# Kernel optimization log

Hardware: AMD Instinct MI355X
Metric: run time of the kernel (lower is better)

## Reference

```python
import jax, jax.numpy as jnp
import numpy as np

N_NODES = 100000
N_EDGES = 3200000
FEAT = 256
HIDDEN = 32
EMBED = 16


def gcn_conv(x, row, col, ew, W, b, num_nodes):
    """PyG GCNConv (add_self_loops=True, normalize=True) in eval mode.
    x: [N, Fin], row/col: [E] (source, target), ew: [E], W: [Fout, Fin], b: [Fout].
    """
    # add self loops with weight 1 (fill_value=1.0)
    loop = jnp.arange(num_nodes, dtype=row.dtype)
    row_f = jnp.concatenate([row, loop])
    col_f = jnp.concatenate([col, loop])
    ew_f = jnp.concatenate([ew, jnp.ones((num_nodes,), dtype=ew.dtype)])
    # symmetric normalization: deg over target (col) for source_to_target flow
    deg = jax.ops.segment_sum(ew_f, col_f, num_segments=num_nodes)
    dis = jnp.where(deg > 0, jax.lax.rsqrt(deg), 0.0)  # deg^{-1/2}, inf -> 0
    norm = dis[row_f] * ew_f * dis[col_f]  # [E+N]
    h = x @ W.T  # [N, Fout] -- linear (no bias) before propagate
    msg = h[row_f] * norm[:, None]  # gather + weight messages
    out = jax.ops.segment_sum(msg, col_f, num_segments=num_nodes)  # scatter-add
    return out + b


def setup_inputs() -> dict:
    key = jax.random.key(0)
    ks = jax.random.split(key, 8)
    x = jax.random.normal(ks[0], (N_NODES, FEAT), dtype=jnp.float32)
    ei = jax.random.randint(ks[1], (2, N_EDGES), 0, N_NODES, dtype=jnp.int64)
    ew = jax.random.uniform(ks[2], (N_EDGES,), dtype=jnp.float32)
    s1 = 1.0 / np.sqrt(FEAT)
    s2 = 1.0 / np.sqrt(HIDDEN)
    W1 = jax.random.uniform(ks[3], (HIDDEN, FEAT), minval=-s1, maxval=s1, dtype=jnp.float32)
    b1 = jax.random.uniform(ks[4], (HIDDEN,), minval=-s1, maxval=s1, dtype=jnp.float32)
    W2 = jax.random.uniform(ks[5], (EMBED, HIDDEN), minval=-s2, maxval=s2, dtype=jnp.float32)
    b2 = jax.random.uniform(ks[6], (EMBED,), minval=-s2, maxval=s2, dtype=jnp.float32)
    return {"x": x, "ei": ei, "ew": ew, "W1": W1, "b1": b1, "W2": W2, "b2": b2}


def reference(x, ei, ew, W1, b1, W2, b2):
    row, col = ei[0], ei[1]
    h = gcn_conv(x, row, col, ew, W1, b1, N_NODES)
    h = jax.nn.relu(h)
    # Dropout(0.25) and DropEdge(0.8) are identity in eval mode
    return gcn_conv(h, row, col, ew, W2, b2, N_NODES)
```

## Files before the change

### kernel.cpp

```cpp
#include <hip/hip_runtime.h>
#include <hip/hip_bf16.h>

#define N_NODES 100000
#define N_EDGES 3200000
#define FEAT 256
#define HIDDEN 32
#define EMBED 16
#define NPB 128
#define NBIN ((N_NODES + NPB - 1) / NPB)
#define CAPB 4608
#define OCAP 8192
#define GR 128
#define G1N 32
#define G1CAP 2048
#define G2N 64
#define G2CAP 3072
#define PEPB 3072
#define PBLK ((N_EDGES + PEPB - 1) / PEPB)
#define OMS 784
#define RPT 5
#define NSK (NPB * 8)

__global__ void k_zero(int* __restrict__ ocur) {
    if (threadIdx.x == 0 && blockIdx.x == 0) *ocur = 0;
}

__global__ __launch_bounds__(256, 4) void k_part(
        const int* __restrict__ row, const int* __restrict__ col,
        const float* __restrict__ ew, int* __restrict__ offm,
        int2* __restrict__ chunks) {
    __shared__ int2 sed[PEPB];
    __shared__ int shist[NBIN];
    __shared__ int scur[NBIN];
    const int tid = threadIdx.x;
    const int blk = blockIdx.x;
    const int e0 = blk * PEPB;
    const int ne = min(PEPB, N_EDGES - e0);

    for (int i = tid; i < NBIN; i += 256) shist[i] = 0;
    __syncthreads();
    for (int i = tid; i < ne; i += 256) atomicAdd(&shist[col[e0 + i] >> 7], 1);
    __syncthreads();
    int l[4];
    int s = 0;
#pragma unroll
    for (int k = 0; k < 4; ++k) {
        int b = tid * 4 + k;
        l[k] = (b < NBIN) ? shist[b] : 0;
        s += l[k];
    }
    scur[tid] = s;
    __syncthreads();
    for (int d = 1; d < 256; d <<= 1) {
        int t = (tid >= d) ? scur[tid - d] : 0;
        __syncthreads();
        scur[tid] += t;
        __syncthreads();
    }
    int ex = scur[tid] - s;
    __syncthreads();
#pragma unroll
    for (int k = 0; k < 4; ++k) {
        int b = tid * 4 + k;
        if (b < NBIN) {
            shist[b] = ex;
            scur[b] = ex;
            ex += l[k];
        }
    }
    __syncthreads();
    for (int b = tid; b < NBIN; b += 256) offm[blk * OMS + b] = shist[b];
    if (tid == 0) offm[blk * OMS + NBIN] = ne;
    for (int i = tid; i < ne; i += 256) {
        int e = e0 + i;
        int c = col[e];
        int b = c >> 7;
        int p = atomicAdd(&scur[b], 1);
        sed[p] = make_int2(((c & (NPB - 1)) << 17) | row[e], __float_as_int(ew[e]));
    }
    __syncthreads();
    for (int i = tid; i < ne; i += 256) chunks[(size_t)blk * PEPB + i] = sed[i];
}

__global__ __launch_bounds__(256) void k_build(
        const int* __restrict__ offm, const int2* __restrict__ chunks,
        int2* __restrict__ binned, float* __restrict__ deg,
        int2* __restrict__ off2, int* __restrict__ binTot,
        int* __restrict__ ocur, int4* __restrict__ olist) {
    __shared__ int2 se[CAPB];
    __shared__ int scnt[NSK], scur2[NSK];
    __shared__ float sdeg[NPB];
    __shared__ int spart[256];
    const int bin = blockIdx.x, tid = threadIdx.x;
    const size_t base = (size_t)bin * CAPB;

    for (int i = tid; i < NSK; i += 256) scnt[i] = 0;
    for (int i = tid; i < NPB; i += 256) sdeg[i] = 0.f;
    int st[RPT], ln[RPT];
    int s = 0;
#pragma unroll
    for (int r = 0; r < RPT; ++r) {
        int k = tid * RPT + r;
        int a = 0, b2 = 0;
        if (k < PBLK) {
            a = offm[k * OMS + bin];
            b2 = offm[k * OMS + bin + 1];
        }
        st[r] = a;
        ln[r] = b2 - a;
        s += ln[r];
    }
    spart[tid] = s;
    __syncthreads();
    for (int d = 1; d < 256; d <<= 1) {
        int t = (tid >= d) ? spart[tid - d] : 0;
        __syncthreads();
        spart[tid] += t;
        __syncthreads();
    }
    int ex = spart[tid] - s;
    const int nTot = spart[255];
    const int n = min(nTot, CAPB);
    int dp = ex;
#pragma unroll
    for (int r = 0; r < RPT; ++r) {
        int k = tid * RPT + r;
        if (k < PBLK) {
            const int2* src = chunks + (size_t)k * PEPB + st[r];
            for (int j = 0; j < ln[r]; ++j) {
                int2 v = src[j];
                int lc = v.x >> 17;
                int dst = dp + j;
                if (dst < CAPB) {
                    se[dst] = v;
                    atomicAdd(&scnt[lc * 8 + ((v.x & 0x1FFFF) >> 14)], 1);
                    atomicAdd(&sdeg[lc], __int_as_float(v.y));
                } else {
                    int q = atomicAdd(ocur, 1);
                    if (q < OCAP)
                        olist[q] = make_int4(v.x & 0x1FFFF, bin * NPB + lc, v.y, 0);
                }
            }
            dp += ln[r];
        }
    }
    __syncthreads();
    int l0 = scnt[tid * 4], l1 = scnt[tid * 4 + 1],
        l2 = scnt[tid * 4 + 2], l3 = scnt[tid * 4 + 3];
    int s2 = l0 + l1 + l2 + l3;
    spart[tid] = s2;
    __syncthreads();
    for (int d = 1; d < 256; d <<= 1) {
        int t = (tid >= d) ? spart[tid - d] : 0;
        __syncthreads();
        spart[tid] += t;
        __syncthreads();
    }
    int ex2 = spart[tid] - s2;
    scnt[tid * 4] = ex2;
    scnt[tid * 4 + 1] = ex2 + l0;
    scnt[tid * 4 + 2] = ex2 + l0 + l1;
    scnt[tid * 4 + 3] = ex2 + l0 + l1 + l2;
    __syncthreads();
    for (int i = tid; i < NSK; i += 256) scur2[i] = scnt[i];
    __syncthreads();
    if (tid < NPB) {
        int node = bin * NPB + tid;
        if (node < N_NODES) {
            int stn = scnt[tid * 8];
            int en = (tid == NPB - 1) ? n : scnt[(tid + 1) * 8];
            off2[node] = make_int2((int)base + stn, en - stn);
            deg[node] = sdeg[tid] + 1.0f;
        }
    }
    if (tid == 0) binTot[bin] = n;
    __syncthreads();
    for (int i = tid; i < n; i += 256) {
        int2 v = se[i];
        int lc = v.x >> 17, src2 = v.x & 0x1FFFF;
        int p = atomicAdd(&scur2[lc * 8 + (src2 >> 14)], 1);
        binned[base + p] = make_int2(src2, v.y);
    }
}

__global__ void k_degover(const int* __restrict__ ocur, const int4* __restrict__ olist,
                          float* __restrict__ deg) {
    int p = blockIdx.x * blockDim.x + threadIdx.x;
    int n = min(*ocur, OCAP);
    if (p < n) { int4 t = olist[p]; unsafeAtomicAdd(&deg[t.y], __int_as_float(t.z)); }
}

__global__ void k_dis(float* __restrict__ deg) {
    int i = blockIdx.x * blockDim.x + threadIdx.x;
    if (i < N_NODES) {
        float d = deg[i];
        deg[i] = (d > 0.0f) ? rsqrtf(d) : 0.0f;
    }
}

__global__ void k_wnorm(const int* __restrict__ binTot, int2* __restrict__ csr,
                        const float* __restrict__ dis) {
    int bin = blockIdx.x;
    int n = binTot[bin];
    size_t base = (size_t)bin * CAPB;
    for (int i = threadIdx.x; i < n; i += 256) {
        int2 v = csr[base + i];
        float w = __int_as_float(v.y) * dis[v.x];
        csr[base + i] = make_int2(v.x, __float_as_int(w));
    }
}

__global__ __launch_bounds__(256) void k_gemm1(
        const float* __restrict__ x, const float* __restrict__ W1,
        float* __restrict__ h) {
    __shared__ float sx[GR][36];
    __shared__ float sw[HIDDEN][260];

    const int tid = threadIdx.x;
    const size_t base = (size_t)blockIdx.x * GR;
    const float4* x4 = (const float4*)x;
    const float4* w4 = (const float4*)W1;
    const int rs = tid >> 3;
    const int ks = tid & 7;

    for (int i = tid; i < HIDDEN * 64; i += 256) {
        int f = i >> 6, kq = i & 63;
        *(float4*)&sw[f][kq * 4] = w4[f * 64 + kq];
    }
    float4 stg[4];
#pragma unroll
    for (int m = 0; m < 4; ++m) {
        int rr = rs + 32 * m;
        stg[m] = make_float4(0.f, 0.f, 0.f, 0.f);
        if (base + rr < N_NODES) stg[m] = x4[(base + rr) * 64 + ks];
    }
#pragma unroll
    for (int m = 0; m < 4; ++m) *(float4*)&sx[rs + 32 * m][ks * 4] = stg[m];
    __syncthreads();

    const int r0 = tid >> 3;
    const int c0 = tid & 7;
    float acc[4][4] = {};

    for (int p = 0; p < 8; ++p) {
        if (p < 7) {
#pragma unroll
            for (int m = 0; m < 4; ++m) {
                int rr = rs + 32 * m;
                stg[m] = make_float4(0.f, 0.f, 0.f, 0.f);
                if (base + rr < N_NODES) stg[m] = x4[(base + rr) * 64 + (p + 1) * 8 + ks];
            }
        }
#pragma unroll
        for (int kq = 0; kq < 8; ++kq) {
            float4 xa[4], wv[4];
#pragma unroll
            for (int m = 0; m < 4; ++m) xa[m] = *(const float4*)&sx[r0 + 32 * m][kq * 4];
#pragma unroll
            for (int j = 0; j < 4; ++j) wv[j] = *(const float4*)&sw[c0 + 8 * j][(p * 8 + kq) * 4];
#pragma unroll
            for (int m = 0; m < 4; ++m)
#pragma unroll
                for (int j = 0; j < 4; ++j)
                    acc[m][j] += xa[m].x * wv[j].x + xa[m].y * wv[j].y +
                                 xa[m].z * wv[j].z + xa[m].w * wv[j].w;
        }
        __syncthreads();
        if (p < 7) {
#pragma unroll
            for (int m = 0; m < 4; ++m) *(float4*)&sx[rs + 32 * m][ks * 4] = stg[m];
            __syncthreads();
        }
    }

#pragma unroll
    for (int m = 0; m < 4; ++m) {
        size_t r = base + r0 + 32 * m;
        if (r < N_NODES) {
#pragma unroll
            for (int j = 0; j < 4; ++j) h[r * HIDDEN + c0 + 8 * j] = acc[m][j];
        }
    }
}

__global__ __launch_bounds__(256) void k_gather1(
        const int2* __restrict__ off2, const int2* __restrict__ csr,
        const float* __restrict__ h, const float* __restrict__ dis,
        const float* __restrict__ b1, float* __restrict__ out1) {
    __shared__ int2 sc[G1CAP];
    __shared__ int s_start, s_n;
    const int tid = threadIdx.x;
    const int node0 = blockIdx.x * G1N;
    if (tid == 0) {
        int2 a = off2[node0];
        int2 b = off2[node0 + G1N - 1];
        s_start = a.x;
        s_n = b.x + b.y - a.x;
    }
    __syncthreads();
    const int start = s_start, n = s_n;
    const bool fit = (n <= G1CAP);
    if (fit) for (int i = tid; i < n; i += 256) sc[i] = csr[start + i];
    __syncthreads();

    const int node = node0 + (tid >> 3);
    const int og = tid & 7;
    float d = dis[node];
    float d2 = d * d;
    float4 self = *(const float4*)(h + (size_t)node * HIDDEN + og * 4);
    float4 bv = *(const float4*)(b1 + og * 4);
    float4 acc = make_float4(0.f, 0.f, 0.f, 0.f);

    int2 o = off2[node];
    for (int j = 0; j < o.y; ++j) {
        int2 v = fit ? sc[o.x - start + j] : csr[o.x + j];
        float w = __int_as_float(v.y);
        const float4 hv = *(const float4*)(h + (size_t)v.x * HIDDEN + og * 4);
        acc.x += hv.x * w; acc.y += hv.y * w; acc.z += hv.z * w; acc.w += hv.w * w;
    }
    *(float4*)(out1 + (size_t)node * HIDDEN + og * 4) =
        make_float4(acc.x * d + self.x * d2 + bv.x, acc.y * d + self.y * d2 + bv.y,
                    acc.z * d + self.z * d2 + bv.z, acc.w * d + self.w * d2 + bv.w);
}

__global__ void k_over1(const int* __restrict__ ocur, const int4* __restrict__ olist,
                        const float* __restrict__ dis, const float* __restrict__ h,
                        float* __restrict__ out1) {
    int p = blockIdx.x * blockDim.x + threadIdx.x;
    int n = min(*ocur, OCAP);
    if (p < n) {
        int4 t = olist[p];
        int r = t.x, c = t.y;
        float w = dis[r] * __int_as_float(t.z) * dis[c];
        for (int f = 0; f < HIDDEN; ++f)
            unsafeAtomicAdd(&out1[(size_t)c * HIDDEN + f], h[(size_t)r * HIDDEN + f] * w);
    }
}

__global__ void k_gemm2(const float* __restrict__ out1, const float* __restrict__ W2,
                        float* __restrict__ h2) {
    int t = blockIdx.x * blockDim.x + threadIdx.x;
    int i = t >> 4;
    if (i >= N_NODES) return;
    int f = t & 15;
    const float* r = out1 + (size_t)i * HIDDEN;
    const float* w = W2 + f * HIDDEN;
    float acc = 0.f;
#pragma unroll
    for (int k = 0; k < HIDDEN; ++k) acc += fmaxf(r[k], 0.f) * w[k];
    h2[(size_t)i * EMBED + f] = acc;
}

__global__ __launch_bounds__(256) void k_gather2(
        const int2* __restrict__ off2, const int2* __restrict__ csr,
        const float* __restrict__ h2, const float* __restrict__ dis,
        const float* __restrict__ b2, float* __restrict__ out) {
    __shared__ int2 sc[G2CAP];
    __shared__ int s_start, s_n;
    const int tid = threadIdx.x;
    const int node0 = blockIdx.x * G2N;
    const int lastn = min(node0 + G2N, N_NODES) - 1;
    if (tid == 0) {
        int2 a = off2[node0];
        int2 b = off2[lastn];
        s_start = a.x;
        s_n = b.x + b.y - a.x;
    }
    __syncthreads();
    const int start = s_start, n = s_n;
    const bool fit = (n <= G2CAP);
    if (fit) for (int i = tid; i < n; i += 256) sc[i] = csr[start + i];
    __syncthreads();

    const int node = node0 + (tid >> 2);
    const int og = tid & 3;
    if (node >= N_NODES) return;
    float d = dis[node];
    float d2 = d * d;
    float4 self = *(const float4*)(h2 + (size_t)node * EMBED + og * 4);
    float4 bv = *(const float4*)(b2 + og * 4);
    float4 acc = make_float4(0.f, 0.f, 0.f, 0.f);

    int2 o = off2[node];
    for (int j = 0; j < o.y; ++j) {
        int2 v = fit ? sc[o.x - start + j] : csr[o.x + j];
        float w = __int_as_float(v.y);
        const float4 hv = *(const float4*)(h2 + (size_t)v.x * EMBED + og * 4);
        acc.x += hv.x * w; acc.y += hv.y * w; acc.z += hv.z * w; acc.w += hv.w * w;
    }
    *(float4*)(out + (size_t)node * EMBED + og * 4) =
        make_float4(acc.x * d + self.x * d2 + bv.x, acc.y * d + self.y * d2 + bv.y,
                    acc.z * d + self.z * d2 + bv.z, acc.w * d + self.w * d2 + bv.w);
}

__global__ void k_over2(const int* __restrict__ ocur, const int4* __restrict__ olist,
                        const float* __restrict__ dis, const float* __restrict__ h2,
                        float* __restrict__ out) {
    int p = blockIdx.x * blockDim.x + threadIdx.x;
    int n = min(*ocur, OCAP);
    if (p < n) {
        int4 t = olist[p];
        int r = t.x, c = t.y;
        float w = dis[r] * __int_as_float(t.z) * dis[c];
        for (int f = 0; f < EMBED; ++f)
            unsafeAtomicAdd(&out[(size_t)c * EMBED + f], h2[(size_t)r * EMBED + f] * w);
    }
}

extern "C" void kernel_launch(void* const* d_in, const int* in_sizes, int n_in,
                              void* d_out, int out_size, void* d_ws, size_t ws_size,
                              hipStream_t stream) {
    const float* x  = (const float*)d_in[0];
    const int*   ei = (const int*)d_in[1];
    const float* ew = (const float*)d_in[2];
    const float* W1 = (const float*)d_in[3];
    const float* b1 = (const float*)d_in[4];
    const float* W2 = (const float*)d_in[5];
    const float* b2 = (const float*)d_in[6];
    float* out = (float*)d_out;

    const int* row = ei;
    const int* col = ei + N_EDGES;

    int2*  off2   = (int2*)d_ws;
    int2*  binned = off2 + N_NODES;
    float* deg    = (float*)(binned + (size_t)NBIN * CAPB);
    int*   binTot = (int*)(deg + N_NODES);
    int*   offm   = binTot + 784;
    int*   ocur   = offm + (size_t)PBLK * OMS;
    int4*  olist  = (int4*)(ocur + 4);
    void*  big    = (void*)(olist + OCAP);
    int2*  chunks = (int2*)big;
    float* h      = (float*)big;
    float* out1   = h + (size_t)N_NODES * HIDDEN;
    float* h2     = h;

    const int B = 256;
    const int gN = (N_NODES + B - 1) / B;
    const int gO = (OCAP + B - 1) / B;

    k_zero<<<1, 64, 0, stream>>>(ocur);
    k_part<<<PBLK, B, 0, stream>>>(row, col, ew, offm, chunks);
    k_build<<<NBIN, B, 0, stream>>>(offm, chunks, binned, deg, off2, binTot, ocur, olist);
    k_degover<<<gO, B, 0, stream>>>(ocur, olist, deg);
    k_dis<<<gN, B, 0, stream>>>(deg);
    k_wnorm<<<NBIN, B, 0, stream>>>(binTot, binned, deg);
    k_gemm1<<<(N_NODES + GR - 1) / GR, B, 0, stream>>>(x, W1, h);
    k_gather1<<<N_NODES / G1N, B, 0, stream>>>(off2, binned, h, deg, b1, out1);
    k_over1<<<gO, B, 0, stream>>>(ocur, olist, deg, h, out1);
    k_gemm2<<<(N_NODES * 16 + B - 1) / B, B, 0, stream>>>(out1, W2, h2);
    k_gather2<<<(N_NODES + G2N - 1) / G2N, B, 0, stream>>>(off2, binned, h2, deg, b2, out);
    k_over2<<<gO, B, 0, stream>>>(ocur, olist, deg, h2, out);
}
```

Measured before the change: 329.1 us.

## Fuse overflow edges, ReLU and second GEMM into gather kernels

Layer 1's gather kernel now adds the overflow-list edges itself, applies ReLU, and multiplies by W2 through shared memory to write h2 directly. This removes the out1 round trip and the separate overflow-atomic and gemm2 launches. Layer 2's gather also folds in the overflow edges, so k_over2 is gone. In exchange, every thread scans the whole overflow list linearly whenever it is non-empty, which could be expensive if the list is large.

```diff
diff --git a/kernel.cpp b/kernel.cpp
--- a/kernel.cpp
+++ b/kernel.cpp
@@ -286,9 +286,13 @@
 __global__ __launch_bounds__(256) void k_gather1(
         const int2* __restrict__ off2, const int2* __restrict__ csr,
         const float* __restrict__ h, const float* __restrict__ dis,
-        const float* __restrict__ b1, float* __restrict__ out1) {
+        const float* __restrict__ b1, const float* __restrict__ W2,
+        const int* __restrict__ ocur, const int4* __restrict__ olist,
+        float* __restrict__ h2) {
     __shared__ int2 sc[G1CAP];
-    __shared__ int s_start, s_n;
+    __shared__ float sw2[EMBED][HIDDEN];
+    __shared__ float sout[G1N][HIDDEN + 1];
+    __shared__ int s_start, s_n, s_ov;
     const int tid = threadIdx.x;
     const int node0 = blockIdx.x * G1N;
     if (tid == 0) {
@@ -296,9 +300,11 @@
         int2 b = off2[node0 + G1N - 1];
         s_start = a.x;
         s_n = b.x + b.y - a.x;
-    }
-    __syncthreads();
-    const int start = s_start, n = s_n;
+        s_ov = *ocur;
+    }
+    if (tid < 128) ((float4*)sw2)[tid] = ((const float4*)W2)[tid];
+    __syncthreads();
+    const int start = s_start, n = s_n, ov = min(s_ov, OCAP);
     const bool fit = (n <= G1CAP);
     if (fit) for (int i = tid; i < n; i += 256) sc[i] = csr[start + i];
     __syncthreads();
@@ -318,45 +324,45 @@
         const float4 hv = *(const float4*)(h + (size_t)v.x * HIDDEN + og * 4);
         acc.x += hv.x * w; acc.y += hv.y * w; acc.z += hv.z * w; acc.w += hv.w * w;
     }
-    *(float4*)(out1 + (size_t)node * HIDDEN + og * 4) =
-        make_float4(acc.x * d + self.x * d2 + bv.x, acc.y * d + self.y * d2 + bv.y,
-                    acc.z * d + self.z * d2 + bv.z, acc.w * d + self.w * d2 + bv.w);
-}
-
-__global__ void k_over1(const int* __restrict__ ocur, const int4* __restrict__ olist,
-                        const float* __restrict__ dis, const float* __restrict__ h,
-                        float* __restrict__ out1) {
-    int p = blockIdx.x * blockDim.x + threadIdx.x;
-    int n = min(*ocur, OCAP);
-    if (p < n) {
-        int4 t = olist[p];
-        int r = t.x, c = t.y;
-        float w = dis[r] * __int_as_float(t.z) * dis[c];
-        for (int f = 0; f < HIDDEN; ++f)
-            unsafeAtomicAdd(&out1[(size_t)c * HIDDEN + f], h[(size_t)r * HIDDEN + f] * w);
-    }
-}
-
-__global__ void k_gemm2(const float* __restrict__ out1, const float* __restrict__ W2,
-                        float* __restrict__ h2) {
-    int t = blockIdx.x * blockDim.x + threadIdx.x;
-    int i = t >> 4;
-    if (i >= N_NODES) return;
-    int f = t & 15;
-    const float* r = out1 + (size_t)i * HIDDEN;
-    const float* w = W2 + f * HIDDEN;
-    float acc = 0.f;
-#pragma unroll
-    for (int k = 0; k < HIDDEN; ++k) acc += fmaxf(r[k], 0.f) * w[k];
-    h2[(size_t)i * EMBED + f] = acc;
+    float4 res = make_float4(acc.x * d + self.x * d2 + bv.x,
+                             acc.y * d + self.y * d2 + bv.y,
+                             acc.z * d + self.z * d2 + bv.z,
+                             acc.w * d + self.w * d2 + bv.w);
+    if (ov > 0) {
+        for (int q = 0; q < ov; ++q) {
+            int4 t = olist[q];
+            if (t.y == node) {
+                float w = dis[t.x] * __int_as_float(t.z) * d;
+                const float4 hv = *(const float4*)(h + (size_t)t.x * HIDDEN + og * 4);
+                res.x += hv.x * w; res.y += hv.y * w;
+                res.z += hv.z * w; res.w += hv.w * w;
+            }
+        }
+    }
+    *(float4*)&sout[tid >> 3][og * 4] =
+        make_float4(fmaxf(res.x, 0.f), fmaxf(res.y, 0.f),
+                    fmaxf(res.z, 0.f), fmaxf(res.w, 0.f));
+    __syncthreads();
+    const int n2 = tid >> 3;
+    const int f2 = (tid & 7) * 2;
+    float a0 = 0.f, a1 = 0.f;
+#pragma unroll
+    for (int k = 0; k < HIDDEN; ++k) {
+        float r = sout[n2][k];
+        a0 += r * sw2[f2][k];
+        a1 += r * sw2[f2 + 1][k];
+    }
+    h2[(size_t)(node0 + n2) * EMBED + f2] = a0;
+    h2[(size_t)(node0 + n2) * EMBED + f2 + 1] = a1;
 }
 
 __global__ __launch_bounds__(256) void k_gather2(
         const int2* __restrict__ off2, const int2* __restrict__ csr,
         const float* __restrict__ h2, const float* __restrict__ dis,
-        const float* __restrict__ b2, float* __restrict__ out) {
+        const float* __restrict__ b2, const int* __restrict__ ocur,
+        const int4* __restrict__ olist, float* __restrict__ out) {
     __shared__ int2 sc[G2CAP];
-    __shared__ int s_start, s_n;
+    __shared__ int s_start, s_n, s_ov;
     const int tid = threadIdx.x;
     const int node0 = blockIdx.x * G2N;
     const int lastn = min(node0 + G2N, N_NODES) - 1;
@@ -365,9 +371,10 @@
         int2 b = off2[lastn];
         s_start = a.x;
         s_n = b.x + b.y - a.x;
-    }
-    __syncthreads();
-    const int start = s_start, n = s_n;
+        s_ov = *ocur;
+    }
+    __syncthreads();
+    const int start = s_start, n = s_n, ov = min(s_ov, OCAP);
     const bool fit = (n <= G2CAP);
     if (fit) for (int i = tid; i < n; i += 256) sc[i] = csr[start + i];
     __syncthreads();
@@ -388,23 +395,22 @@
         const float4 hv = *(const float4*)(h2 + (size_t)v.x * EMBED + og * 4);
         acc.x += hv.x * w; acc.y += hv.y * w; acc.z += hv.z * w; acc.w += hv.w * w;
     }
-    *(float4*)(out + (size_t)node * EMBED + og * 4) =
-        make_float4(acc.x * d + self.x * d2 + bv.x, acc.y * d + self.y * d2 + bv.y,
-                    acc.z * d + self.z * d2 + bv.z, acc.w * d + self.w * d2 + bv.w);
-}
-
-__global__ void k_over2(const int* __restrict__ ocur, const int4* __restrict__ olist,
-                        const float* __restrict__ dis, const float* __restrict__ h2,
-                        float* __restrict__ out) {
-    int p = blockIdx.x * blockDim.x + threadIdx.x;
-    int n = min(*ocur, OCAP);
-    if (p < n) {
-        int4 t = olist[p];
-        int r = t.x, c = t.y;
-        float w = dis[r] * __int_as_float(t.z) * dis[c];
-        for (int f = 0; f < EMBED; ++f)
-            unsafeAtomicAdd(&out[(size_t)c * EMBED + f], h2[(size_t)r * EMBED + f] * w);
-    }
+    float4 res = make_float4(acc.x * d + self.x * d2 + bv.x,
+                             acc.y * d + self.y * d2 + bv.y,
+                             acc.z * d + self.z * d2 + bv.z,
+                             acc.w * d + self.w * d2 + bv.w);
+    if (ov > 0) {
+        for (int q = 0; q < ov; ++q) {
+            int4 t = olist[q];
+            if (t.y == node) {
+                float w = dis[t.x] * __int_as_float(t.z) * d;
+                const float4 hv = *(const float4*)(h2 + (size_t)t.x * EMBED + og * 4);
+                res.x += hv.x * w; res.y += hv.y * w;
+                res.z += hv.z * w; res.w += hv.w * w;
+            }
+        }
+    }
+    *(float4*)(out + (size_t)node * EMBED + og * 4) = res;
 }
 
 extern "C" void kernel_launch(void* const* d_in, const int* in_sizes, int n_in,
@@ -432,8 +438,7 @@
     void*  big    = (void*)(olist + OCAP);
     int2*  chunks = (int2*)big;
     float* h      = (float*)big;
-    float* out1   = h + (size_t)N_NODES * HIDDEN;
-    float* h2     = h;
+    float* h2     = h + (size_t)N_NODES * HIDDEN;
 
     const int B = 256;
     const int gN = (N_NODES + B - 1) / B;
@@ -446,9 +451,6 @@
     k_dis<<<gN, B, 0, stream>>>(deg);
     k_wnorm<<<NBIN, B, 0, stream>>>(binTot, binned, deg);
     k_gemm1<<<(N_NODES + GR - 1) / GR, B, 0, stream>>>(x, W1, h);
-    k_gather1<<<N_NODES / G1N, B, 0, stream>>>(off2, binned, h, deg, b1, out1);
-    k_over1<<<gO, B, 0, stream>>>(ocur, olist, deg, h, out1);
-    k_gemm2<<<(N_NODES * 16 + B - 1) / B, B, 0, stream>>>(out1, W2, h2);
-    k_gather2<<<(N_NODES + G2N - 1) / G2N, B, 0, stream>>>(off2, binned, h2, deg, b2, out);
-    k_over2<<<gO, B, 0, stream>>>(ocur, olist, deg, h2, out);
-}
+    k_gather1<<<N_NODES / G1N, B, 0, stream>>>(off2, binned, h, deg, b1, W2, ocur, olist, h2);
+    k_gather2<<<(N_NODES + G2N - 1) / G2N, B, 0, stream>>>(off2, binned, h2, deg, b2, ocur, olist, out);
+}
```

Result: faster. 307.2 us (-6.7%).
